# Performance work log

Hardware: AMD Instinct MI355X
Metric: run time of the kernel (lower is better)

The kernel has to match this reference:

```python
import jax, jax.numpy as jnp
import numpy as np

FS = 4            # filter_size
DIV_FLOW = 20.0   # PWCNet flow scale
T = 0.5           # timestep


def _upsample4(flow, H, W):
    # nn.Upsample(scale_factor=4, mode='bilinear', align_corners=False)
    B, C = flow.shape[0], flow.shape[1]
    return jax.image.resize(flow, (B, C, H, W), method='bilinear')


def _flow_project(flow):
    """DAIN FlowProjection: forward-scatter -flow to the 4 integer neighbors of
    (x+fx, y+fy), average by hit count, fill holes with valid 4-neighbor mean."""
    B, _, H, W = flow.shape
    gx = jnp.arange(W, dtype=flow.dtype)[None, None, :]
    gy = jnp.arange(H, dtype=flow.dtype)[None, :, None]
    x2 = gx + flow[:, 0]
    y2 = gy + flow[:, 1]
    valid = (x2 >= 0) & (x2 <= W - 1) & (y2 >= 0) & (y2 <= H - 1)
    xf = jnp.floor(x2).astype(jnp.int32)
    yf = jnp.floor(y2).astype(jnp.int32)
    vfx = jnp.where(valid, -flow[:, 0], 0.0).reshape(-1)
    vfy = jnp.where(valid, -flow[:, 1], 0.0).reshape(-1)
    vc = valid.astype(flow.dtype).reshape(-1)
    boff = (jnp.arange(B, dtype=jnp.int32) * (H * W))[:, None, None]
    accx = jnp.zeros(B * H * W, flow.dtype)
    accy = jnp.zeros(B * H * W, flow.dtype)
    cnt = jnp.zeros(B * H * W, flow.dtype)
    for dy in (0, 1):
        for dx in (0, 1):
            xi = jnp.clip(xf + dx, 0, W - 1)
            yi = jnp.clip(yf + dy, 0, H - 1)
            idx = (boff + yi * W + xi).reshape(-1)
            accx = accx.at[idx].add(vfx)
            accy = accy.at[idx].add(vfy)
            cnt = cnt.at[idx].add(vc)
    cnt = cnt.reshape(B, H, W)
    avg = jnp.stack([accx.reshape(B, H, W), accy.reshape(B, H, W)], axis=1)
    avg = avg / jnp.maximum(cnt, 1.0)[:, None]
    hole = cnt <= 0                       # (B,H,W)
    ok = (~hole).astype(flow.dtype)[:, None]
    fp = jnp.pad(avg * ok, ((0, 0), (0, 0), (1, 1), (1, 1)))
    op = jnp.pad(ok, ((0, 0), (0, 0), (1, 1), (1, 1)))
    num = fp[:, :, :-2, 1:-1] + fp[:, :, 2:, 1:-1] + fp[:, :, 1:-1, :-2] + fp[:, :, 1:-1, 2:]
    den = op[:, :, :-2, 1:-1] + op[:, :, 2:, 1:-1] + op[:, :, 1:-1, :-2] + op[:, :, 1:-1, 2:]
    filled = num / jnp.maximum(den, 1.0)
    return jnp.where(hole[:, None], filled, avg)


def _filter_interp(img, flow, filt, fs):
    """DAIN FilterInterpolation: out(p) = sum_{j,i} filt[j*fs+i,p] *
    bilinear(img, p + flow + (i+1-fs/2, j+1-fs/2))."""
    B, C, H, W = img.shape
    gx = jnp.arange(W, dtype=img.dtype)[None, None, :]
    gy = jnp.arange(H, dtype=img.dtype)[None, :, None]
    x2 = jnp.clip(gx + flow[:, 0], 0.0, W - 1.0)
    y2 = jnp.clip(gy + flow[:, 1], 0.0, H - 1.0)
    xf = jnp.floor(x2).astype(jnp.int32)
    yf = jnp.floor(y2).astype(jnp.int32)
    a = (x2 - xf)[:, None]   # (B,1,H,W)
    b = (y2 - yf)[:, None]
    w00 = (1.0 - a) * (1.0 - b)
    w10 = a * (1.0 - b)
    w01 = (1.0 - a) * b
    w11 = a * b
    flat = img.reshape(B, C, H * W)

    def gather(yi, xi):
        idx = (yi * W + xi).reshape(B, 1, H * W)
        return jnp.take_along_axis(flat, idx, axis=2).reshape(B, C, H, W)

    off = 1 - fs // 2
    out = jnp.zeros_like(img)
    for j in range(fs):
        yT = jnp.clip(yf + j + off, 0, H - 1)
        yB = jnp.clip(yf + j + off + 1, 0, H - 1)
        for i in range(fs):
            xL = jnp.clip(xf + i + off, 0, W - 1)
            xR = jnp.clip(xf + i + off + 1, 0, W - 1)
            v = (w00 * gather(yT, xL) + w10 * gather(yT, xR)
                 + w01 * gather(yB, xL) + w11 * gather(yB, xR))
            out = out + v * filt[:, j * fs + i][:, None]
    return out


def setup_inputs() -> dict:
    key = jax.random.key(0)
    k = jax.random.split(key, 6)
    B, H, W = 4, 384, 512
    return {
        'input0': jax.random.uniform(k[0], (B, 3, H, W), jnp.float32),
        'input2': jax.random.uniform(k[1], (B, 3, H, W), jnp.float32),
        'flow01': jax.random.normal(k[2], (B, 2, H // 4, W // 4), jnp.float32),
        'flow10': jax.random.normal(k[3], (B, 2, H // 4, W // 4), jnp.float32),
        'filt0': jax.random.uniform(k[4], (B, FS * FS, H, W), jnp.float32),
        'filt1': jax.random.uniform(k[5], (B, FS * FS, H, W), jnp.float32),
    }


def reference(input0, input2, flow01, flow10, filt0, filt1):
    B, _, H, W = input0.shape
    scale = DIV_FLOW * T
    f01 = _upsample4(flow01 * scale, H, W)   # F_{0->2} scaled to t=0.5
    f10 = _upsample4(flow10 * scale, H, W)   # F_{2->0} scaled to t=0.5
    Ft0 = _flow_project(f01)                 # F_{t->0}
    Ft2 = _flow_project(f10)                 # F_{t->2}
    ref0 = _filter_interp(input0, Ft0, filt0, FS)
    ref2 = _filter_interp(input2, Ft2, filt1, FS)
    return 0.5 * (ref0 + ref2)
```

## Files before the change

kernel.cpp:

```cpp
#include <hip/hip_runtime.h>

#define HH 384
#define WW 512
#define NB 4
#define HWP (HH * WW)
#define NPIX (NB * HWP)
#define SH 96
#define SW 128
#define SHW (SH * SW)

#define MBOUND 24
#define BAND 4
#define NBANDS (HH / BAND)
#define NROWS (BAND + 3)
#define OV_CAP 131072

static __device__ __forceinline__ float upsample_flow_f32(const float* __restrict__ f, int y, int x) {
    float sx = __fadd_rn(__fmul_rn((float)x, 0.25f), -0.375f);
    float sy = __fadd_rn(__fmul_rn((float)y, 0.25f), -0.375f);
    float fx0 = floorf(sx), fy0 = floorf(sy);
    float wx = __fsub_rn(sx, fx0);
    float wy = __fsub_rn(sy, fy0);
    int ix = (int)fx0, iy = (int)fy0;
    int x0 = max(ix, 0), x1 = min(ix + 1, SW - 1);
    int y0 = max(iy, 0), y1 = min(iy + 1, SH - 1);
    float v00 = __fmul_rn(10.0f, f[y0 * SW + x0]);
    float v01 = __fmul_rn(10.0f, f[y0 * SW + x1]);
    float v10 = __fmul_rn(10.0f, f[y1 * SW + x0]);
    float v11 = __fmul_rn(10.0f, f[y1 * SW + x1]);
    float omx = __fsub_rn(1.0f, wx);
    float omy = __fsub_rn(1.0f, wy);
    float w00 = __fmul_rn(omx, omy);
    float w10 = __fmul_rn(wx, omy);
    float w01 = __fmul_rn(omx, wy);
    float w11 = __fmul_rn(wx, wy);
    float s = __fmul_rn(w00, v00);
    s = __fadd_rn(s, __fmul_rn(w10, v01));
    s = __fadd_rn(s, __fmul_rn(w01, v10));
    s = __fadd_rn(s, __fmul_rn(w11, v11));
    return s;
}

__global__ __launch_bounds__(256) void upsample_k(const float* __restrict__ flow01,
                                                  const float* __restrict__ flow10,
                                                  float* __restrict__ Fu, float* __restrict__ ovf) {
    int idx = blockIdx.x * blockDim.x + threadIdx.x;
    if (idx >= NPIX) return;
    int side = blockIdx.y;
    const float* flow = side ? flow10 : flow01;
    int x = idx % WW;
    int y = (idx / WW) % HH;
    int b = idx / HWP;
    const float* fp = flow + b * 2 * SHW;
    float fx = upsample_flow_f32(fp, y, x);
    float fy = upsample_flow_f32(fp + SHW, y, x);
    float* F = Fu + side * 2 * NPIX;
    F[idx] = fx;
    F[NPIX + idx] = fy;
    float x2 = __fadd_rn((float)x, fx);
    float y2 = __fadd_rn((float)y, fy);
    bool valid = (x2 >= 0.0f && x2 <= (float)(WW - 1) && y2 >= 0.0f && y2 <= (float)(HH - 1));
    bool banded = (fy >= -(float)MBOUND && fy < (float)MBOUND);
    if (valid && !banded) {
        int xf = (int)floorf(x2);
        int yf = (int)floorf(y2);
        int key = side * NPIX + b * HWP + yf * WW + xf;
        int slot = atomicAdd((int*)ovf, 1);
        if (slot >= 0 && slot < OV_CAP) {
            ((int*)ovf)[64 + slot] = key;
            ovf[64 + OV_CAP + slot] = -fx;
            ovf[64 + 2 * OV_CAP + slot] = -fy;
        }
    }
}

static __device__ __forceinline__ void box_sum_lds(const float (&acc)[3][NROWS][WW], int rbase,
                                                   int y, int x, float& ax, float& ay, float& c) {
    float wxs1 = (x == WW - 1) ? 2.0f : 1.0f;
    float wys1 = (y == HH - 1) ? 2.0f : 1.0f;
    float sx = 0.0f, sy = 0.0f, sc = 0.0f;
    #pragma unroll
    for (int j = 0; j < 2; j++) {
        int ey = y - 1 + j;
        if (ey < 0) continue;
        float wy = j ? wys1 : 1.0f;
        int rr = ey - rbase;
        #pragma unroll
        for (int i = 0; i < 2; i++) {
            int ex = x - 1 + i;
            if (ex < 0) continue;
            float w = wy * ((i ? wxs1 : 1.0f));
            sx += w * acc[0][rr][ex];
            sy += w * acc[1][rr][ex];
            sc += w * acc[2][rr][ex];
        }
    }
    ax = sx; ay = sy; c = sc;
}

__global__ __launch_bounds__(512, 6) void rgf_interp_k(const float* __restrict__ Fu,
                                                       const float* __restrict__ ovf,
                                                       const float* __restrict__ img0,
                                                       const float* __restrict__ img2,
                                                       const float* __restrict__ filt0,
                                                       const float* __restrict__ filt1,
                                                       float* __restrict__ out) {
    __shared__ float acc[3][NROWS][WW];
    int bid = blockIdx.x;
    int slab = bid & 7;
    int side = slab >> 2;
    int b = slab & 3;
    int t0 = (bid >> 3) * BAND;
    int rbase = t0 - 2;

    const float* Fx = Fu + side * 2 * NPIX + b * HWP;
    const float* Fyp = Fx + NPIX;

    float* A = &acc[0][0][0];
    for (int k = threadIdx.x; k < 3 * NROWS * WW; k += 512) A[k] = 0.0f;
    __syncthreads();

    int sLo = max(t0 - 2 - (MBOUND - 1), 0);
    int sHi = min(t0 + BAND + MBOUND, HH - 1);
    int nitems = (sHi - sLo + 1) * 128;
    for (int k = threadIdx.x; k < nitems; k += 512) {
        int s = sLo + (k >> 7);
        int tx = k & 127;
        int rowoff = s * WW + 4 * tx;
        float4 fxv = *(const float4*)(Fx + rowoff);
        float4 fyv = *(const float4*)(Fyp + rowoff);
        float sf = (float)s;
        #pragma unroll
        for (int u = 0; u < 4; ++u) {
            int xx = 4 * tx + u;
            float fx = (u == 0) ? fxv.x : (u == 1) ? fxv.y : (u == 2) ? fxv.z : fxv.w;
            float fy = (u == 0) ? fyv.x : (u == 1) ? fyv.y : (u == 2) ? fyv.z : fyv.w;
            float x2 = __fadd_rn((float)xx, fx);
            float y2 = __fadd_rn(sf, fy);
            if (x2 >= 0.0f && x2 <= (float)(WW - 1) && y2 >= 0.0f && y2 <= (float)(HH - 1)
                && fy >= -(float)MBOUND && fy < (float)MBOUND) {
                int yf = (int)floorf(y2);
                int r = yf - rbase;
                if (r >= 0 && r < NROWS) {
                    int xf = (int)floorf(x2);
                    atomicAdd(&acc[0][r][xf], -fx);
                    atomicAdd(&acc[1][r][xf], -fy);
                    atomicAdd(&acc[2][r][xf], 1.0f);
                }
            }
        }
    }

    int n = ((const int*)ovf)[0];
    n = (n < 0) ? 0 : ((n > OV_CAP) ? OV_CAP : n);
    int lo = max(rbase, 0) * WW;
    int hi = (min(t0 + BAND, HH - 1) + 1) * WW;
    int keybase = side * NPIX + b * HWP;
    for (int i = threadIdx.x; i < n; i += 512) {
        int rel = ((const int*)ovf)[64 + i] - keybase;
        if (rel >= lo && rel < hi) {
            int r = rel / WW - rbase;
            int xf = rel % WW;
            atomicAdd(&acc[0][r][xf], ovf[64 + OV_CAP + i]);
            atomicAdd(&acc[1][r][xf], ovf[64 + 2 * OV_CAP + i]);
            atomicAdd(&acc[2][r][xf], 1.0f);
        }
    }
    __syncthreads();

    const float* img  = side ? img2  : img0;
    const float* filt = side ? filt1 : filt0;
    int x = threadIdx.x;

    for (int j = 0; j < BAND; ++j) {
        int y = t0 + j;

        float ax, ay, c;
        box_sum_lds(acc, rbase, y, x, ax, ay, c);
        float fx, fy;
        if (c > 0.0f) {
            fx = ax / c;
            fy = ay / c;
        } else {
            float nx = 0.0f, ny = 0.0f, den = 0.0f;
            float bx, by, bc;
            if (y > 0)      { box_sum_lds(acc, rbase, y - 1, x, bx, by, bc); if (bc > 0.0f) { nx += bx / bc; ny += by / bc; den += 1.0f; } }
            if (y < HH - 1) { box_sum_lds(acc, rbase, y + 1, x, bx, by, bc); if (bc > 0.0f) { nx += bx / bc; ny += by / bc; den += 1.0f; } }
            if (x > 0)      { box_sum_lds(acc, rbase, y, x - 1, bx, by, bc); if (bc > 0.0f) { nx += bx / bc; ny += by / bc; den += 1.0f; } }
            if (x < WW - 1) { box_sum_lds(acc, rbase, y, x + 1, bx, by, bc); if (bc > 0.0f) { nx += bx / bc; ny += by / bc; den += 1.0f; } }
            float inv = 1.0f / fmaxf(den, 1.0f);
            fx = nx * inv;
            fy = ny * inv;
        }

        float x2 = fminf(fmaxf((float)x + fx, 0.0f), (float)(WW - 1));
        float y2 = fminf(fmaxf((float)y + fy, 0.0f), (float)(HH - 1));
        float xff = floorf(x2), yff = floorf(y2);
        int xf = (int)xff, yf = (int)yff;
        float a  = x2 - xff;
        float bb = y2 - yff;
        float w00 = (1.0f - a) * (1.0f - bb);
        float w10 = a * (1.0f - bb);
        float w01 = (1.0f - a) * bb;
        float w11 = a * bb;

        float F[4][4];
        #pragma unroll
        for (int k = 0; k < 16; k++) {
            F[k >> 2][k & 3] = filt[((b * 16 + k) * HH + y) * WW + x];
        }
        float Cf[5][5];
        #pragma unroll
        for (int r = 0; r < 5; r++) {
            #pragma unroll
            for (int sc = 0; sc < 5; sc++) {
                float v = 0.0f;
                if (r < 4 && sc < 4)   v += w00 * F[r][sc];
                if (r < 4 && sc >= 1)  v += w10 * F[r][sc - 1];
                if (r >= 1 && sc < 4)  v += w01 * F[r - 1][sc];
                if (r >= 1 && sc >= 1) v += w11 * F[r - 1][sc - 1];
                Cf[r][sc] = v;
            }
        }
        int rows[5];
        #pragma unroll
        for (int r = 0; r < 5; r++) rows[r] = min(max(yf - 1 + r, 0), HH - 1);

        bool interior = (xf >= 1) && (xf <= WW - 4);
        if (interior) {
            int x0 = xf - 1;
            #pragma unroll
            for (int ch = 0; ch < 3; ch++) {
                const float* ip = img + (b * 3 + ch) * HWP;
                float accv = 0.0f;
                #pragma unroll
                for (int r = 0; r < 5; r++) {
                    const float* rp = ip + rows[r] * WW + x0;
                    float wrow[5];
                    __builtin_memcpy(wrow, rp, 5 * sizeof(float));
                    #pragma unroll
                    for (int sc = 0; sc < 5; sc++) {
                        accv += Cf[r][sc] * wrow[sc];
                    }
                }
                unsafeAtomicAdd(&out[((b * 3 + ch) * HH + y) * WW + x], 0.5f * accv);
            }
        } else {
            int cols[5];
            #pragma unroll
            for (int sc = 0; sc < 5; sc++) cols[sc] = min(max(xf - 1 + sc, 0), WW - 1);
            #pragma unroll
            for (int ch = 0; ch < 3; ch++) {
                const float* ip = img + (b * 3 + ch) * HWP;
                float accv = 0.0f;
                #pragma unroll
                for (int r = 0; r < 5; r++) {
                    const float* rp = ip + rows[r] * WW;
                    #pragma unroll
                    for (int sc = 0; sc < 5; sc++) {
                        accv += Cf[r][sc] * rp[cols[sc]];
                    }
                }
                unsafeAtomicAdd(&out[((b * 3 + ch) * HH + y) * WW + x], 0.5f * accv);
            }
        }
    }
}

extern "C" void kernel_launch(void* const* d_in, const int* in_sizes, int n_in,
                              void* d_out, int out_size, void* d_ws, size_t ws_size,
                              hipStream_t stream) {
    const float* input0 = (const float*)d_in[0];
    const float* input2 = (const float*)d_in[1];
    const float* flow01 = (const float*)d_in[2];
    const float* flow10 = (const float*)d_in[3];
    const float* filt0  = (const float*)d_in[4];
    const float* filt1  = (const float*)d_in[5];
    float* out = (float*)d_out;

    float* ws = (float*)d_ws;
    float* Fu   = ws;
    float* ovf  = ws + 4 * NPIX;

    const int BS = 256;
    const int NBLK = (NPIX + BS - 1) / BS;

    hipMemsetAsync(out, 0, (size_t)3 * NPIX * sizeof(float), stream);
    hipMemsetAsync(ovf, 0, 256, stream);

    upsample_k<<<dim3(NBLK, 2), BS, 0, stream>>>(flow01, flow10, Fu, ovf);
    rgf_interp_k<<<dim3(2 * NB * NBANDS), 512, 0, stream>>>(
        Fu, ovf, input0, input2, filt0, filt1, out);
}
```

Measured before the change: 267.2 us.

## Compute four upsampled pixels per thread, widen row bands, relax occupancy bound

The upsample kernel now has each thread produce four horizontally adjacent output pixels. It shares the coarse-grid loads and row weights across them and writes the result with float4 stores. The interpolation kernel's band height goes from 4 to 6 rows, which reduces the redundant halo and source-scan work per output row but raises LDS use per block. The min-blocks hint in launch_bounds is also dropped, which may change register allocation and occupancy.

```diff
diff --git a/kernel.cpp b/kernel.cpp
--- a/kernel.cpp
+++ b/kernel.cpp
@@ -10,66 +10,89 @@
 #define SHW (SH * SW)
 
 #define MBOUND 24
-#define BAND 4
+#define BAND 6
 #define NBANDS (HH / BAND)
 #define NROWS (BAND + 3)
 #define OV_CAP 131072
 
-static __device__ __forceinline__ float upsample_flow_f32(const float* __restrict__ f, int y, int x) {
-    float sx = __fadd_rn(__fmul_rn((float)x, 0.25f), -0.375f);
-    float sy = __fadd_rn(__fmul_rn((float)y, 0.25f), -0.375f);
-    float fx0 = floorf(sx), fy0 = floorf(sy);
-    float wx = __fsub_rn(sx, fx0);
-    float wy = __fsub_rn(sy, fy0);
-    int ix = (int)fx0, iy = (int)fy0;
-    int x0 = max(ix, 0), x1 = min(ix + 1, SW - 1);
-    int y0 = max(iy, 0), y1 = min(iy + 1, SH - 1);
-    float v00 = __fmul_rn(10.0f, f[y0 * SW + x0]);
-    float v01 = __fmul_rn(10.0f, f[y0 * SW + x1]);
-    float v10 = __fmul_rn(10.0f, f[y1 * SW + x0]);
-    float v11 = __fmul_rn(10.0f, f[y1 * SW + x1]);
-    float omx = __fsub_rn(1.0f, wx);
-    float omy = __fsub_rn(1.0f, wy);
-    float w00 = __fmul_rn(omx, omy);
-    float w10 = __fmul_rn(wx, omy);
-    float w01 = __fmul_rn(omx, wy);
-    float w11 = __fmul_rn(wx, wy);
-    float s = __fmul_rn(w00, v00);
-    s = __fadd_rn(s, __fmul_rn(w10, v01));
-    s = __fadd_rn(s, __fmul_rn(w01, v10));
-    s = __fadd_rn(s, __fmul_rn(w11, v11));
-    return s;
-}
-
-__global__ __launch_bounds__(256) void upsample_k(const float* __restrict__ flow01,
-                                                  const float* __restrict__ flow10,
-                                                  float* __restrict__ Fu, float* __restrict__ ovf) {
-    int idx = blockIdx.x * blockDim.x + threadIdx.x;
-    if (idx >= NPIX) return;
+__global__ __launch_bounds__(256) void upsample4_k(const float* __restrict__ flow01,
+                                                   const float* __restrict__ flow10,
+                                                   float* __restrict__ Fu, float* __restrict__ ovf) {
+    int q = blockIdx.x * blockDim.x + threadIdx.x;
+    if (q >= NPIX / 4) return;
     int side = blockIdx.y;
     const float* flow = side ? flow10 : flow01;
-    int x = idx % WW;
-    int y = (idx / WW) % HH;
-    int b = idx / HWP;
+    int k = q % (WW / 4);
+    int y = (q / (WW / 4)) % HH;
+    int b = q / ((WW / 4) * HH);
     const float* fp = flow + b * 2 * SHW;
-    float fx = upsample_flow_f32(fp, y, x);
-    float fy = upsample_flow_f32(fp + SHW, y, x);
+
+    float sy = __fadd_rn(__fmul_rn((float)y, 0.25f), -0.375f);
+    float fy0 = floorf(sy);
+    float wy = __fsub_rn(sy, fy0);
+    int iy = (int)fy0;
+    int y0 = max(iy, 0), y1 = min(iy + 1, SH - 1);
+    float omy = __fsub_rn(1.0f, wy);
+
+    int cm1 = max(k - 1, 0);
+    int cp1 = min(k + 1, SW - 1);
+
+    const float wxs[4]  = {0.625f, 0.875f, 0.125f, 0.375f};
+    float res[2][4];
+
+    #pragma unroll
+    for (int comp = 0; comp < 2; ++comp) {
+        const float* f = fp + comp * SHW;
+        float a0 = __fmul_rn(10.0f, f[y0 * SW + cm1]);
+        float a1 = __fmul_rn(10.0f, f[y0 * SW + k]);
+        float a2 = __fmul_rn(10.0f, f[y0 * SW + cp1]);
+        float b0 = __fmul_rn(10.0f, f[y1 * SW + cm1]);
+        float b1 = __fmul_rn(10.0f, f[y1 * SW + k]);
+        float b2 = __fmul_rn(10.0f, f[y1 * SW + cp1]);
+        #pragma unroll
+        for (int u = 0; u < 4; ++u) {
+            float v00 = (u < 2) ? a0 : a1;
+            float v01 = (u < 2) ? a1 : a2;
+            float v10 = (u < 2) ? b0 : b1;
+            float v11 = (u < 2) ? b1 : b2;
+            float wx = wxs[u];
+            float omx = __fsub_rn(1.0f, wx);
+            float w00 = __fmul_rn(omx, omy);
+            float w10 = __fmul_rn(wx, omy);
+            float w01 = __fmul_rn(omx, wy);
+            float w11 = __fmul_rn(wx, wy);
+            float s = __fmul_rn(w00, v00);
+            s = __fadd_rn(s, __fmul_rn(w10, v01));
+            s = __fadd_rn(s, __fmul_rn(w01, v10));
+            s = __fadd_rn(s, __fmul_rn(w11, v11));
+            res[comp][u] = s;
+        }
+    }
+
+    int idx = b * HWP + y * WW + 4 * k;
     float* F = Fu + side * 2 * NPIX;
-    F[idx] = fx;
-    F[NPIX + idx] = fy;
-    float x2 = __fadd_rn((float)x, fx);
-    float y2 = __fadd_rn((float)y, fy);
-    bool valid = (x2 >= 0.0f && x2 <= (float)(WW - 1) && y2 >= 0.0f && y2 <= (float)(HH - 1));
-    bool banded = (fy >= -(float)MBOUND && fy < (float)MBOUND);
-    if (valid && !banded) {
-        int xf = (int)floorf(x2);
-        int yf = (int)floorf(y2);
-        int key = side * NPIX + b * HWP + yf * WW + xf;
-        int slot = atomicAdd((int*)ovf, 1);
-        if (slot >= 0 && slot < OV_CAP) {
-            ((int*)ovf)[64 + slot] = key;
-            ovf[64 + OV_CAP + slot] = -fx;
-            ovf[64 + 2 * OV_CAP + slot] = -fy;
+    *(float4*)(F + idx)        = make_float4(res[0][0], res[0][1], res[0][2], res[0][3]);
+    *(float4*)(F + NPIX + idx) = make_float4(res[1][0], res[1][1], res[1][2], res[1][3]);
+
+    #pragma unroll
+    for (int u = 0; u < 4; ++u) {
+        float fx = res[0][u];
+        float fy = res[1][u];
+        int x = 4 * k + u;
+        float x2 = __fadd_rn((float)x, fx);
+        float y2 = __fadd_rn((float)y, fy);
+        bool valid = (x2 >= 0.0f && x2 <= (float)(WW - 1) && y2 >= 0.0f && y2 <= (float)(HH - 1));
+        bool banded = (fy >= -(float)MBOUND && fy < (float)MBOUND);
+        if (valid && !banded) {
+            int xf = (int)floorf(x2);
+            int yf = (int)floorf(y2);
+            int key = side * NPIX + b * HWP + yf * WW + xf;
+            int slot = atomicAdd((int*)ovf, 1);
+            if (slot >= 0 && slot < OV_CAP) {
+                ((int*)ovf)[64 + slot] = key;
+                ovf[64 + OV_CAP + slot] = -fx;
+                ovf[64 + 2 * OV_CAP + slot] = -fy;
+            }
         }
     }
 }
@@ -98,13 +121,13 @@
     ax = sx; ay = sy; c = sc;
 }
 
-__global__ __launch_bounds__(512, 6) void rgf_interp_k(const float* __restrict__ Fu,
-                                                       const float* __restrict__ ovf,
-                                                       const float* __restrict__ img0,
-                                                       const float* __restrict__ img2,
-                                                       const float* __restrict__ filt0,
-                                                       const float* __restrict__ filt1,
-                                                       float* __restrict__ out) {
+__global__ __launch_bounds__(512) void rgf_interp_k(const float* __restrict__ Fu,
+                                                    const float* __restrict__ ovf,
+                                                    const float* __restrict__ img0,
+                                                    const float* __restrict__ img2,
+                                                    const float* __restrict__ filt0,
+                                                    const float* __restrict__ filt1,
+                                                    float* __restrict__ out) {
     __shared__ float acc[3][NROWS][WW];
     int bid = blockIdx.x;
     int slab = bid & 7;
@@ -283,12 +306,12 @@
     float* ovf  = ws + 4 * NPIX;
 
     const int BS = 256;
-    const int NBLK = (NPIX + BS - 1) / BS;
+    const int NQBLK = (NPIX / 4 + BS - 1) / BS;
 
     hipMemsetAsync(out, 0, (size_t)3 * NPIX * sizeof(float), stream);
     hipMemsetAsync(ovf, 0, 256, stream);
 
-    upsample_k<<<dim3(NBLK, 2), BS, 0, stream>>>(flow01, flow10, Fu, ovf);
+    upsample4_k<<<dim3(NQBLK, 2), BS, 0, stream>>>(flow01, flow10, Fu, ovf);
     rgf_interp_k<<<dim3(2 * NB * NBANDS), 512, 0, stream>>>(
         Fu, ovf, input0, input2, filt0, filt1, out);
 }
```

After: 254.6 us. 4.7% less time.
